# Kernel optimization log

Hardware: AMD Instinct MI355X
Metric: run time of the kernel (lower is better)

Reference implementation:

```python
import jax, jax.numpy as jnp
import numpy as np


def setup_inputs() -> dict:
    key = jax.random.key(0)
    ks = jax.random.split(key, 8)
    n_videos, emb_dim = 200000, 128
    n_nodes, k_neigh = 20000, 32
    sc = 1.0 / np.sqrt(emb_dim)
    return {
        "video_embeddings": jax.random.normal(ks[0], (n_videos, emb_dim), jnp.float32),
        "video_nodes": jax.random.randint(ks[1], (n_nodes,), 0, n_videos, jnp.int64 if jax.config.jax_enable_x64 else jnp.int32),
        "neigh_idx": jax.random.randint(ks[2], (n_nodes, k_neigh), 0, n_videos, jnp.int64 if jax.config.jax_enable_x64 else jnp.int32),
        "W1": jax.random.normal(ks[3], (2 * emb_dim, emb_dim), jnp.float32) * sc,
        "b1": jnp.zeros((emb_dim,), jnp.float32),
        "W2": jax.random.normal(ks[4], (emb_dim, emb_dim), jnp.float32) * sc,
        "b2": jnp.zeros((emb_dim,), jnp.float32),
        "W3": jax.random.normal(ks[5], (emb_dim, 1), jnp.float32) * sc,
        "b3": jnp.zeros((1,), jnp.float32),
    }


def reference(video_embeddings, video_nodes, neigh_idx, W1, b1, W2, b2, W3, b3):
    # Ragged per-node loop vectorized as a padded [N, K] neighbor gather.
    neigh_emb = video_embeddings[neigh_idx]          # [N, K, D]
    node_emb = video_embeddings[video_nodes]         # [N, D]
    n, k, d = neigh_emb.shape
    # Attention MLP: cat(neigh, node_repeated) -> relu -> relu -> scalar score
    x = jnp.concatenate([neigh_emb, jnp.broadcast_to(node_emb[:, None, :], (n, k, d))], axis=-1)  # [N, K, 2D]
    h = jax.nn.relu(jnp.einsum("nke,ed->nkd", x, W1) + b1)
    h = jax.nn.relu(jnp.einsum("nke,ed->nkd", h, W2) + b2)
    scores = (jnp.einsum("nkd,do->nko", h, W3) + b3)[..., 0]  # [N, K]
    att = jax.nn.softmax(scores, axis=-1)                      # softmax over neighbors
    # Weighted aggregation: embed_matrix[i] = neigh_emb[i].T @ att[i]
    return jnp.einsum("nkd,nk->nd", neigh_emb, att)
```

## Files before the change

### kernel.cpp

```cpp
#include <hip/hip_runtime.h>
#include <hip/hip_bf16.h>

#define D  128
#define KN 32
#define LST 136

typedef __attribute__((ext_vector_type(8))) short bf16x8;
typedef __attribute__((ext_vector_type(4))) float f32x4;

static __device__ __forceinline__ unsigned short f2bf(float f) {
    union { float f; unsigned int u; } v; v.f = f;
    unsigned int u = v.u;
    u += 0x7fff + ((u >> 16) & 1);
    return (unsigned short)(u >> 16);
}
static __device__ __forceinline__ float bf2f(unsigned short h) {
    union { float f; unsigned int u; } v; v.u = ((unsigned int)h) << 16;
    return v.f;
}
static __device__ __forceinline__ unsigned int pk2bf(float a, float b) {
    float2 t; t.x = a; t.y = b;
    __hip_bfloat162 h = __float22bfloat162_rn(t);
    union { __hip_bfloat162 h; unsigned int u; } v; v.h = h;
    return v.u;
}

__global__ __launch_bounds__(256) void wt_kernel(
    const float* __restrict__ W1, const float* __restrict__ W2,
    unsigned short* __restrict__ W1Tt, unsigned short* __restrict__ W1Tb,
    unsigned short* __restrict__ W2T)
{
    int idx = blockIdx.x * 256 + threadIdx.x;
    if (idx < D * D) {
        int col = idx >> 7, e = idx & 127;
        W1Tt[col * D + e] = f2bf(W1[e * D + col]);
        W1Tb[col * D + e] = f2bf(W1[(D + e) * D + col]);
        W2T [col * D + e] = f2bf(W2[e * D + col]);
    }
}

__global__ __launch_bounds__(256) void q_kernel(
    const float* __restrict__ emb, const int* __restrict__ vnodes, int NN,
    const unsigned short* __restrict__ W1Tb, const float* __restrict__ b1,
    float* __restrict__ Qf)
{
    __shared__ unsigned short sA[128][LST];

    const int tid  = threadIdx.x;
    const int lane = tid & 63;
    const int w    = tid >> 6;
    const int m    = lane & 15, q = lane >> 4;
    const int r0   = blockIdx.x * 128;

#pragma unroll
    for (int i = 0; i < 16; ++i) {
        int e = tid + 256 * i;
        int row = e >> 5, c4 = (e & 31) << 2;
        int r = r0 + row; if (r > NN - 1) r = NN - 1;
        int vr = vnodes[r];
        const float4 f = *(const float4*)(emb + (long)vr * D + c4);
        ushort4 h;
        h.x = f2bf(f.x); h.y = f2bf(f.y); h.z = f2bf(f.z); h.w = f2bf(f.w);
        *(ushort4*)(&sA[row][c4]) = h;
    }
    __syncthreads();

    bf16x8 Bf[2][4];
#pragma unroll
    for (int nt = 0; nt < 2; ++nt)
#pragma unroll
        for (int kk = 0; kk < 4; ++kk)
            Bf[nt][kk] = *(const bf16x8*)(W1Tb + (32 * w + 16 * nt + m) * D + kk * 32 + q * 8);
    float bv[2];
#pragma unroll
    for (int nt = 0; nt < 2; ++nt) bv[nt] = b1[32 * w + 16 * nt + m];

    f32x4 acc[8][2];
#pragma unroll
    for (int mt = 0; mt < 8; ++mt)
#pragma unroll
        for (int nt = 0; nt < 2; ++nt) acc[mt][nt] = (f32x4){0.f, 0.f, 0.f, 0.f};

#pragma unroll
    for (int kk = 0; kk < 4; ++kk)
#pragma unroll
        for (int mt = 0; mt < 8; ++mt) {
            bf16x8 a = *(const bf16x8*)(&sA[16 * mt + m][kk * 32 + q * 8]);
            acc[mt][0] = __builtin_amdgcn_mfma_f32_16x16x32_bf16(a, Bf[0][kk], acc[mt][0], 0, 0, 0);
            acc[mt][1] = __builtin_amdgcn_mfma_f32_16x16x32_bf16(a, Bf[1][kk], acc[mt][1], 0, 0, 0);
        }

#pragma unroll
    for (int mt = 0; mt < 8; ++mt)
#pragma unroll
        for (int nt = 0; nt < 2; ++nt) {
            int col = 32 * w + 16 * nt + m;
#pragma unroll
            for (int r = 0; r < 4; ++r) {
                int row = r0 + 16 * mt + 4 * q + r;
                if (row < NN) Qf[(long)row * D + col] = acc[mt][nt][r] + bv[nt];
            }
        }
}

__global__ __launch_bounds__(256, 3) void agg_kernel(
    const float* __restrict__ emb, const int* __restrict__ nidx,
    const unsigned short* __restrict__ W1Tt, const unsigned short* __restrict__ W2T,
    const float* __restrict__ b2, const float* __restrict__ W3,
    const float* __restrict__ b3, const float* __restrict__ Qf,
    float* __restrict__ out, int NN)
{
    __shared__ unsigned short sU[128][LST];
    __shared__ float sQf[4][D];
    __shared__ float sSp[4][128];
    __shared__ float sAtt[128];

    const int tid  = threadIdx.x;
    const int lane = tid & 63;
    const int w    = tid >> 6;
    const int m    = lane & 15, q = lane >> 4;

    bf16x8 Af[2][4], Bf[2][4];
#pragma unroll
    for (int t = 0; t < 2; ++t)
#pragma unroll
        for (int kk = 0; kk < 4; ++kk) {
            Af[t][kk] = *(const bf16x8*)(W1Tt + (32 * w + 16 * t + m) * D + kk * 32 + q * 8);
            Bf[t][kk] = *(const bf16x8*)(W2T  + (32 * w + 16 * t + m) * D + kk * 32 + q * 8);
        }
    float b2v[2], w3v[2];
#pragma unroll
    for (int nt = 0; nt < 2; ++nt) {
        int col = 32 * w + 16 * nt + m;
        b2v[nt] = b2[col];
        w3v[nt] = W3[col];
    }
    const float b3s = b3[0];

    const int groups = (NN + 3) >> 2;
    for (int g = blockIdx.x; g < groups; g += gridDim.x) {
        const int node0 = g * 4;

        {
            int i2 = tid * 2, nd = i2 >> 7, c = i2 & 127;
            int ndg = node0 + nd; if (ndg > NN - 1) ndg = NN - 1;
            *(float2*)(&sQf[nd][c]) = *(const float2*)(Qf + (long)ndg * D + c);
        }
        {
            int row = tid >> 1, half = tid & 1;
            int ndg = node0 + (row >> 5); if (ndg > NN - 1) ndg = NN - 1;
            int ni = nidx[ndg * KN + (row & 31)];
            const float* src = emb + (long)ni * D + half * 64;
#pragma unroll
            for (int j = 0; j < 8; ++j) {
                float4 f0 = *(const float4*)(src + j * 8);
                float4 f1 = *(const float4*)(src + j * 8 + 4);
                uint4 pk;
                pk.x = pk2bf(f0.x, f0.y); pk.y = pk2bf(f0.z, f0.w);
                pk.z = pk2bf(f1.x, f1.y); pk.w = pk2bf(f1.z, f1.w);
                *(uint4*)(&sU[row][half * 64 + j * 8]) = pk;
            }
        }
        __syncthreads();

        bf16x8 gv[8];
#pragma unroll
        for (int j = 0; j < 8; ++j)
            gv[j] = *(const bf16x8*)(&sU[w * KN + (lane >> 4) + 4 * j][(lane & 15) * 8]);

        f32x4 acc1[4][2][2];
#pragma unroll
        for (int nd = 0; nd < 4; ++nd)
#pragma unroll
            for (int t = 0; t < 2; ++t)
#pragma unroll
                for (int nt = 0; nt < 2; ++nt) acc1[nd][t][nt] = (f32x4){0.f, 0.f, 0.f, 0.f};

#pragma unroll
        for (int nd = 0; nd < 4; ++nd)
#pragma unroll
            for (int kk = 0; kk < 4; ++kk) {
                bf16x8 e0 = *(const bf16x8*)(&sU[nd * 32 + m][kk * 32 + q * 8]);
                bf16x8 e1 = *(const bf16x8*)(&sU[nd * 32 + 16 + m][kk * 32 + q * 8]);
                acc1[nd][0][0] = __builtin_amdgcn_mfma_f32_16x16x32_bf16(Af[0][kk], e0, acc1[nd][0][0], 0, 0, 0);
                acc1[nd][1][0] = __builtin_amdgcn_mfma_f32_16x16x32_bf16(Af[1][kk], e0, acc1[nd][1][0], 0, 0, 0);
                acc1[nd][0][1] = __builtin_amdgcn_mfma_f32_16x16x32_bf16(Af[0][kk], e1, acc1[nd][0][1], 0, 0, 0);
                acc1[nd][1][1] = __builtin_amdgcn_mfma_f32_16x16x32_bf16(Af[1][kk], e1, acc1[nd][1][1], 0, 0, 0);
            }
        __syncthreads();

#pragma unroll
        for (int nd = 0; nd < 4; ++nd)
#pragma unroll
            for (int t = 0; t < 2; ++t) {
                int xc = 32 * w + 16 * t + 4 * q;
                float q0 = sQf[nd][xc], q1 = sQf[nd][xc + 1];
                float q2 = sQf[nd][xc + 2], q3 = sQf[nd][xc + 3];
#pragma unroll
                for (int nt = 0; nt < 2; ++nt) {
                    float v0 = fmaxf(acc1[nd][t][nt][0] + q0, 0.f);
                    float v1 = fmaxf(acc1[nd][t][nt][1] + q1, 0.f);
                    float v2 = fmaxf(acc1[nd][t][nt][2] + q2, 0.f);
                    float v3 = fmaxf(acc1[nd][t][nt][3] + q3, 0.f);
                    uint2 pk; pk.x = pk2bf(v0, v1); pk.y = pk2bf(v2, v3);
                    *(uint2*)(&sU[nd * 32 + 16 * nt + m][xc]) = pk;
                }
            }
        __syncthreads();

        f32x4 acc[8][2];
#pragma unroll
        for (int mt = 0; mt < 8; ++mt)
#pragma unroll
            for (int nt = 0; nt < 2; ++nt) acc[mt][nt] = (f32x4){0.f, 0.f, 0.f, 0.f};

#pragma unroll
        for (int kk = 0; kk < 4; ++kk)
#pragma unroll
            for (int mt = 0; mt < 8; ++mt) {
                bf16x8 a = *(const bf16x8*)(&sU[16 * mt + m][kk * 32 + q * 8]);
                acc[mt][0] = __builtin_amdgcn_mfma_f32_16x16x32_bf16(a, Bf[0][kk], acc[mt][0], 0, 0, 0);
                acc[mt][1] = __builtin_amdgcn_mfma_f32_16x16x32_bf16(a, Bf[1][kk], acc[mt][1], 0, 0, 0);
            }

#pragma unroll
        for (int mt = 0; mt < 8; ++mt) {
            float p[4];
#pragma unroll
            for (int r = 0; r < 4; ++r) {
                float h0 = acc[mt][0][r] + b2v[0]; h0 = h0 > 0.f ? h0 : 0.f;
                float h1 = acc[mt][1][r] + b2v[1]; h1 = h1 > 0.f ? h1 : 0.f;
                p[r] = h0 * w3v[0] + h1 * w3v[1];
            }
#pragma unroll
            for (int off = 8; off >= 1; off >>= 1)
#pragma unroll
                for (int r = 0; r < 4; ++r) p[r] += __shfl_xor(p[r], off, 16);
            if (m == 0) {
#pragma unroll
                for (int r = 0; r < 4; ++r) sSp[w][16 * mt + 4 * q + r] = p[r];
            }
        }
        __syncthreads();

        if (tid < 128) {
            float s = sSp[0][tid] + sSp[1][tid] + sSp[2][tid] + sSp[3][tid] + b3s;
            float mx = s;
#pragma unroll
            for (int off = 16; off >= 1; off >>= 1) mx = fmaxf(mx, __shfl_xor(mx, off, 32));
            float e = __expf(s - mx);
            float sum = e;
#pragma unroll
            for (int off = 16; off >= 1; off >>= 1) sum += __shfl_xor(sum, off, 32);
            sAtt[tid] = e / sum;
        }
        __syncthreads();

        {
            float r[8] = {0.f, 0.f, 0.f, 0.f, 0.f, 0.f, 0.f, 0.f};
#pragma unroll
            for (int j = 0; j < 8; ++j) {
                float a = sAtt[w * KN + (lane >> 4) + 4 * j];
#pragma unroll
                for (int h = 0; h < 8; ++h)
                    r[h] += a * bf2f((unsigned short)gv[j][h]);
            }
#pragma unroll
            for (int h = 0; h < 8; ++h) {
                r[h] += __shfl_xor(r[h], 16);
                r[h] += __shfl_xor(r[h], 32);
            }
            int ndw = node0 + w;
            if (lane < 16 && ndw < NN) {
                float4 o0 = {r[0], r[1], r[2], r[3]};
                float4 o1 = {r[4], r[5], r[6], r[7]};
                *(float4*)(out + (long)ndw * D + lane * 8)     = o0;
                *(float4*)(out + (long)ndw * D + lane * 8 + 4) = o1;
            }
        }
    }
}

__global__ __launch_bounds__(128) void naive_kernel(
    const float* __restrict__ emb, const int* __restrict__ vnodes,
    const int* __restrict__ nidx,
    const float* __restrict__ W1, const float* __restrict__ b1,
    const float* __restrict__ W2, const float* __restrict__ b2,
    const float* __restrict__ W3, const float* __restrict__ b3,
    float* __restrict__ out)
{
    __shared__ float sE[KN + 1][D];
    __shared__ float sH[KN][D];
    __shared__ float sH2[KN][D];
    __shared__ float sS[KN];
    __shared__ float sA2[KN];
    const int node = blockIdx.x, tid = threadIdx.x;

    for (int r = 0; r < KN + 1; ++r) {
        int vr = (r < KN) ? nidx[node * KN + r] : vnodes[node];
        sE[r][tid] = emb[(long)vr * D + tid];
    }
    __syncthreads();
    for (int k = 0; k < KN; ++k) {
        float s = b1[tid];
        for (int e = 0; e < D; ++e) s += sE[k][e]  * W1[e * D + tid];
        for (int e = 0; e < D; ++e) s += sE[KN][e] * W1[(D + e) * D + tid];
        sH[k][tid] = s > 0.f ? s : 0.f;
    }
    __syncthreads();
    for (int k = 0; k < KN; ++k) {
        float s = b2[tid];
        for (int e = 0; e < D; ++e) s += sH[k][e] * W2[e * D + tid];
        sH2[k][tid] = s > 0.f ? s : 0.f;
    }
    __syncthreads();
    if (tid < KN) {
        float s = b3[0];
        for (int e = 0; e < D; ++e) s += sH2[tid][e] * W3[e];
        sS[tid] = s;
    }
    __syncthreads();
    if (tid == 0) {
        float mx = sS[0];
        for (int k = 1; k < KN; ++k) mx = fmaxf(mx, sS[k]);
        float sum = 0.f;
        for (int k = 0; k < KN; ++k) { sA2[k] = __expf(sS[k] - mx); sum += sA2[k]; }
        for (int k = 0; k < KN; ++k) sA2[k] /= sum;
    }
    __syncthreads();
    float a = 0.f;
    for (int k = 0; k < KN; ++k) a += sA2[k] * sE[k][tid];
    out[(long)node * D + tid] = a;
}

extern "C" void kernel_launch(void* const* d_in, const int* in_sizes, int n_in,
                              void* d_out, int out_size, void* d_ws, size_t ws_size,
                              hipStream_t stream) {
    const float* emb    = (const float*)d_in[0];
    const int*   vnodes = (const int*)d_in[1];
    const int*   nidx   = (const int*)d_in[2];
    const float* W1     = (const float*)d_in[3];
    const float* b1     = (const float*)d_in[4];
    const float* W2     = (const float*)d_in[5];
    const float* b2     = (const float*)d_in[6];
    const float* W3     = (const float*)d_in[7];
    const float* b3     = (const float*)d_in[8];
    float* out = (float*)d_out;

    const int NN = in_sizes[1];

    const size_t q_bytes  = (size_t)NN * D * sizeof(float);
    const size_t wt_elems = (size_t)D * D;
    const size_t need = q_bytes + 3 * wt_elems * sizeof(unsigned short);

    if (ws_size >= need) {
        float* Qf            = (float*)d_ws;
        unsigned short* W1Tt = (unsigned short*)((char*)d_ws + q_bytes);
        unsigned short* W1Tb = W1Tt + wt_elems;
        unsigned short* W2T  = W1Tb + wt_elems;

        wt_kernel<<<(D * D + 255) / 256, 256, 0, stream>>>(W1, W2, W1Tt, W1Tb, W2T);
        q_kernel<<<(NN + 127) / 128, 256, 0, stream>>>(emb, vnodes, NN, W1Tb, b1, Qf);
        agg_kernel<<<2048, 256, 0, stream>>>(
            emb, nidx, W1Tt, W2T, b2, W3, b3, Qf, out, NN);
    } else {
        naive_kernel<<<NN, D, 0, stream>>>(emb, vnodes, nidx, W1, b1, W2, b2, W3, b3, out);
    }
}
```

Baseline: 336.0 us.

## Process two nodes per block iteration with separate gather and hidden LDS buffers

The aggregation kernel now handles 2 nodes (64 neighbour rows) per loop iteration instead of 4. It keeps the gathered embeddings in their own LDS buffer and writes the layer-1 output to a second buffer, which removes one barrier and the register copy of the gathered rows. The final weighted sum is done by 128 threads reading straight from LDS, and the grid is doubled. The b3 bias is dropped because softmax does not change when a constant is added. Smaller LDS and register use should allow more resident blocks, at the cost of more loop iterations and an extra barrier at the end of each one.

```diff
diff --git a/kernel.cpp b/kernel.cpp
--- a/kernel.cpp
+++ b/kernel.cpp
@@ -14,9 +14,11 @@
     u += 0x7fff + ((u >> 16) & 1);
     return (unsigned short)(u >> 16);
 }
-static __device__ __forceinline__ float bf2f(unsigned short h) {
-    union { float f; unsigned int u; } v; v.u = ((unsigned int)h) << 16;
-    return v.f;
+static __device__ __forceinline__ float bflo(unsigned int u) {
+    union { float f; unsigned int u; } v; v.u = u << 16; return v.f;
+}
+static __device__ __forceinline__ float bfhi(unsigned int u) {
+    union { float f; unsigned int u; } v; v.u = u & 0xffff0000u; return v.f;
 }
 static __device__ __forceinline__ unsigned int pk2bf(float a, float b) {
     float2 t; t.x = a; t.y = b;
@@ -107,13 +109,14 @@
     const float* __restrict__ emb, const int* __restrict__ nidx,
     const unsigned short* __restrict__ W1Tt, const unsigned short* __restrict__ W2T,
     const float* __restrict__ b2, const float* __restrict__ W3,
-    const float* __restrict__ b3, const float* __restrict__ Qf,
+    const float* __restrict__ Qf,
     float* __restrict__ out, int NN)
 {
-    __shared__ unsigned short sU[128][LST];
-    __shared__ float sQf[4][D];
-    __shared__ float sSp[4][128];
-    __shared__ float sAtt[128];
+    __shared__ unsigned short sEg[64][LST];
+    __shared__ unsigned short sX[64][LST];
+    __shared__ float sQf[2][D];
+    __shared__ float sSp[4][64];
+    __shared__ float sAtt[64];
 
     const int tid  = threadIdx.x;
     const int lane = tid & 63;
@@ -135,116 +138,121 @@
         b2v[nt] = b2[col];
         w3v[nt] = W3[col];
     }
-    const float b3s = b3[0];
-
-    const int groups = (NN + 3) >> 2;
+
+    const int groups = (NN + 1) >> 1;
     for (int g = blockIdx.x; g < groups; g += gridDim.x) {
-        const int node0 = g * 4;
+        const int node0 = g * 2;
 
         {
-            int i2 = tid * 2, nd = i2 >> 7, c = i2 & 127;
+            int nd = tid >> 7, c = tid & 127;
             int ndg = node0 + nd; if (ndg > NN - 1) ndg = NN - 1;
-            *(float2*)(&sQf[nd][c]) = *(const float2*)(Qf + (long)ndg * D + c);
+            sQf[nd][c] = Qf[(long)ndg * D + c];
         }
         {
-            int row = tid >> 1, half = tid & 1;
+            int row = tid >> 2, qt = tid & 3;
             int ndg = node0 + (row >> 5); if (ndg > NN - 1) ndg = NN - 1;
             int ni = nidx[ndg * KN + (row & 31)];
-            const float* src = emb + (long)ni * D + half * 64;
-#pragma unroll
-            for (int j = 0; j < 8; ++j) {
-                float4 f0 = *(const float4*)(src + j * 8);
-                float4 f1 = *(const float4*)(src + j * 8 + 4);
-                uint4 pk;
-                pk.x = pk2bf(f0.x, f0.y); pk.y = pk2bf(f0.z, f0.w);
-                pk.z = pk2bf(f1.x, f1.y); pk.w = pk2bf(f1.z, f1.w);
-                *(uint4*)(&sU[row][half * 64 + j * 8]) = pk;
-            }
-        }
-        __syncthreads();
-
-        bf16x8 gv[8];
-#pragma unroll
-        for (int j = 0; j < 8; ++j)
-            gv[j] = *(const bf16x8*)(&sU[w * KN + (lane >> 4) + 4 * j][(lane & 15) * 8]);
-
-        f32x4 acc1[4][2][2];
-#pragma unroll
-        for (int nd = 0; nd < 4; ++nd)
+            const float* src = emb + (long)ni * D + qt * 32;
+            float4 f0 = *(const float4*)(src);
+            float4 f1 = *(const float4*)(src + 4);
+            float4 f2 = *(const float4*)(src + 8);
+            float4 f3 = *(const float4*)(src + 12);
+            float4 f4 = *(const float4*)(src + 16);
+            float4 f5 = *(const float4*)(src + 20);
+            float4 f6 = *(const float4*)(src + 24);
+            float4 f7 = *(const float4*)(src + 28);
+            uint4 p0, p1;
+            p0.x = pk2bf(f0.x, f0.y); p0.y = pk2bf(f0.z, f0.w);
+            p0.z = pk2bf(f1.x, f1.y); p0.w = pk2bf(f1.z, f1.w);
+            p1.x = pk2bf(f2.x, f2.y); p1.y = pk2bf(f2.z, f2.w);
+            p1.z = pk2bf(f3.x, f3.y); p1.w = pk2bf(f3.z, f3.w);
+            *(uint4*)(&sEg[row][qt * 32])     = p0;
+            *(uint4*)(&sEg[row][qt * 32 + 8]) = p1;
+            uint4 p2, p3;
+            p2.x = pk2bf(f4.x, f4.y); p2.y = pk2bf(f4.z, f4.w);
+            p2.z = pk2bf(f5.x, f5.y); p2.w = pk2bf(f5.z, f5.w);
+            p3.x = pk2bf(f6.x, f6.y); p3.y = pk2bf(f6.z, f6.w);
+            p3.z = pk2bf(f7.x, f7.y); p3.w = pk2bf(f7.z, f7.w);
+            *(uint4*)(&sEg[row][qt * 32 + 16]) = p2;
+            *(uint4*)(&sEg[row][qt * 32 + 24]) = p3;
+        }
+        __syncthreads();
+
+        {
+            f32x4 acc1[2][4];
 #pragma unroll
             for (int t = 0; t < 2; ++t)
 #pragma unroll
-                for (int nt = 0; nt < 2; ++nt) acc1[nd][t][nt] = (f32x4){0.f, 0.f, 0.f, 0.f};
-
-#pragma unroll
-        for (int nd = 0; nd < 4; ++nd)
-#pragma unroll
-            for (int kk = 0; kk < 4; ++kk) {
-                bf16x8 e0 = *(const bf16x8*)(&sU[nd * 32 + m][kk * 32 + q * 8]);
-                bf16x8 e1 = *(const bf16x8*)(&sU[nd * 32 + 16 + m][kk * 32 + q * 8]);
-                acc1[nd][0][0] = __builtin_amdgcn_mfma_f32_16x16x32_bf16(Af[0][kk], e0, acc1[nd][0][0], 0, 0, 0);
-                acc1[nd][1][0] = __builtin_amdgcn_mfma_f32_16x16x32_bf16(Af[1][kk], e0, acc1[nd][1][0], 0, 0, 0);
-                acc1[nd][0][1] = __builtin_amdgcn_mfma_f32_16x16x32_bf16(Af[0][kk], e1, acc1[nd][0][1], 0, 0, 0);
-                acc1[nd][1][1] = __builtin_amdgcn_mfma_f32_16x16x32_bf16(Af[1][kk], e1, acc1[nd][1][1], 0, 0, 0);
-            }
-        __syncthreads();
-
-#pragma unroll
-        for (int nd = 0; nd < 4; ++nd)
+                for (int nt = 0; nt < 4; ++nt) acc1[t][nt] = (f32x4){0.f, 0.f, 0.f, 0.f};
+
+#pragma unroll
+            for (int kk = 0; kk < 4; ++kk)
+#pragma unroll
+                for (int nt = 0; nt < 4; ++nt) {
+                    bf16x8 e = *(const bf16x8*)(&sEg[16 * nt + m][kk * 32 + q * 8]);
+                    acc1[0][nt] = __builtin_amdgcn_mfma_f32_16x16x32_bf16(Af[0][kk], e, acc1[0][nt], 0, 0, 0);
+                    acc1[1][nt] = __builtin_amdgcn_mfma_f32_16x16x32_bf16(Af[1][kk], e, acc1[1][nt], 0, 0, 0);
+                }
+
 #pragma unroll
             for (int t = 0; t < 2; ++t) {
                 int xc = 32 * w + 16 * t + 4 * q;
-                float q0 = sQf[nd][xc], q1 = sQf[nd][xc + 1];
-                float q2 = sQf[nd][xc + 2], q3 = sQf[nd][xc + 3];
-#pragma unroll
-                for (int nt = 0; nt < 2; ++nt) {
-                    float v0 = fmaxf(acc1[nd][t][nt][0] + q0, 0.f);
-                    float v1 = fmaxf(acc1[nd][t][nt][1] + q1, 0.f);
-                    float v2 = fmaxf(acc1[nd][t][nt][2] + q2, 0.f);
-                    float v3 = fmaxf(acc1[nd][t][nt][3] + q3, 0.f);
+                float q0[4];
+#pragma unroll
+                for (int nt = 0; nt < 4; ++nt) {
+                    int n = 16 * nt + m;
+                    int nd = n >> 5;
+                    float v0 = fmaxf(acc1[t][nt][0] + sQf[nd][xc],     0.f);
+                    float v1 = fmaxf(acc1[t][nt][1] + sQf[nd][xc + 1], 0.f);
+                    float v2 = fmaxf(acc1[t][nt][2] + sQf[nd][xc + 2], 0.f);
+                    float v3 = fmaxf(acc1[t][nt][3] + sQf[nd][xc + 3], 0.f);
                     uint2 pk; pk.x = pk2bf(v0, v1); pk.y = pk2bf(v2, v3);
-                    *(uint2*)(&sU[nd * 32 + 16 * nt + m][xc]) = pk;
-                }
-            }
-        __syncthreads();
-
-        f32x4 acc[8][2];
-#pragma unroll
-        for (int mt = 0; mt < 8; ++mt)
-#pragma unroll
-            for (int nt = 0; nt < 2; ++nt) acc[mt][nt] = (f32x4){0.f, 0.f, 0.f, 0.f};
-
-#pragma unroll
-        for (int kk = 0; kk < 4; ++kk)
-#pragma unroll
-            for (int mt = 0; mt < 8; ++mt) {
-                bf16x8 a = *(const bf16x8*)(&sU[16 * mt + m][kk * 32 + q * 8]);
-                acc[mt][0] = __builtin_amdgcn_mfma_f32_16x16x32_bf16(a, Bf[0][kk], acc[mt][0], 0, 0, 0);
-                acc[mt][1] = __builtin_amdgcn_mfma_f32_16x16x32_bf16(a, Bf[1][kk], acc[mt][1], 0, 0, 0);
-            }
-
-#pragma unroll
-        for (int mt = 0; mt < 8; ++mt) {
-            float p[4];
-#pragma unroll
-            for (int r = 0; r < 4; ++r) {
-                float h0 = acc[mt][0][r] + b2v[0]; h0 = h0 > 0.f ? h0 : 0.f;
-                float h1 = acc[mt][1][r] + b2v[1]; h1 = h1 > 0.f ? h1 : 0.f;
-                p[r] = h0 * w3v[0] + h1 * w3v[1];
-            }
-#pragma unroll
-            for (int off = 8; off >= 1; off >>= 1)
-#pragma unroll
-                for (int r = 0; r < 4; ++r) p[r] += __shfl_xor(p[r], off, 16);
-            if (m == 0) {
-#pragma unroll
-                for (int r = 0; r < 4; ++r) sSp[w][16 * mt + 4 * q + r] = p[r];
-            }
-        }
-        __syncthreads();
-
-        if (tid < 128) {
-            float s = sSp[0][tid] + sSp[1][tid] + sSp[2][tid] + sSp[3][tid] + b3s;
+                    *(uint2*)(&sX[n][xc]) = pk;
+                }
+                (void)q0;
+            }
+        }
+        __syncthreads();
+
+        {
+            f32x4 acc[4][2];
+#pragma unroll
+            for (int mt = 0; mt < 4; ++mt)
+#pragma unroll
+                for (int nt = 0; nt < 2; ++nt) acc[mt][nt] = (f32x4){0.f, 0.f, 0.f, 0.f};
+
+#pragma unroll
+            for (int kk = 0; kk < 4; ++kk)
+#pragma unroll
+                for (int mt = 0; mt < 4; ++mt) {
+                    bf16x8 a = *(const bf16x8*)(&sX[16 * mt + m][kk * 32 + q * 8]);
+                    acc[mt][0] = __builtin_amdgcn_mfma_f32_16x16x32_bf16(a, Bf[0][kk], acc[mt][0], 0, 0, 0);
+                    acc[mt][1] = __builtin_amdgcn_mfma_f32_16x16x32_bf16(a, Bf[1][kk], acc[mt][1], 0, 0, 0);
+                }
+
+#pragma unroll
+            for (int mt = 0; mt < 4; ++mt) {
+                float p[4];
+#pragma unroll
+                for (int r = 0; r < 4; ++r) {
+                    float h0 = acc[mt][0][r] + b2v[0]; h0 = h0 > 0.f ? h0 : 0.f;
+                    float h1 = acc[mt][1][r] + b2v[1]; h1 = h1 > 0.f ? h1 : 0.f;
+                    p[r] = h0 * w3v[0] + h1 * w3v[1];
+                }
+#pragma unroll
+                for (int off = 8; off >= 1; off >>= 1)
+#pragma unroll
+                    for (int r = 0; r < 4; ++r) p[r] += __shfl_xor(p[r], off, 16);
+                if (m == 0) {
+#pragma unroll
+                    for (int r = 0; r < 4; ++r) sSp[w][16 * mt + 4 * q + r] = p[r];
+                }
+            }
+        }
+        __syncthreads();
+
+        if (tid < 64) {
+            float s = sSp[0][tid] + sSp[1][tid] + sSp[2][tid] + sSp[3][tid];
             float mx = s;
 #pragma unroll
             for (int off = 16; off >= 1; off >>= 1) mx = fmaxf(mx, __shfl_xor(mx, off, 32));
@@ -256,28 +264,23 @@
         }
         __syncthreads();
 
-        {
-            float r[8] = {0.f, 0.f, 0.f, 0.f, 0.f, 0.f, 0.f, 0.f};
-#pragma unroll
-            for (int j = 0; j < 8; ++j) {
-                float a = sAtt[w * KN + (lane >> 4) + 4 * j];
-#pragma unroll
-                for (int h = 0; h < 8; ++h)
-                    r[h] += a * bf2f((unsigned short)gv[j][h]);
-            }
-#pragma unroll
-            for (int h = 0; h < 8; ++h) {
-                r[h] += __shfl_xor(r[h], 16);
-                r[h] += __shfl_xor(r[h], 32);
-            }
-            int ndw = node0 + w;
-            if (lane < 16 && ndw < NN) {
-                float4 o0 = {r[0], r[1], r[2], r[3]};
-                float4 o1 = {r[4], r[5], r[6], r[7]};
-                *(float4*)(out + (long)ndw * D + lane * 8)     = o0;
-                *(float4*)(out + (long)ndw * D + lane * 8 + 4) = o1;
-            }
-        }
+        if (tid < 128) {
+            int nd = tid >> 6, c2 = tid & 63;
+            float ox = 0.f, oy = 0.f;
+#pragma unroll
+            for (int k = 0; k < KN; ++k) {
+                float a = sAtt[nd * KN + k];
+                unsigned int v = *(const unsigned int*)(&sEg[nd * KN + k][c2 * 2]);
+                ox += a * bflo(v);
+                oy += a * bfhi(v);
+            }
+            int ndg = node0 + nd;
+            if (ndg < NN) {
+                float2 o = {ox, oy};
+                *(float2*)(out + (long)ndg * D + c2 * 2) = o;
+            }
+        }
+        __syncthreads();
     }
 }
 
@@ -361,8 +364,8 @@
 
         wt_kernel<<<(D * D + 255) / 256, 256, 0, stream>>>(W1, W2, W1Tt, W1Tb, W2T);
         q_kernel<<<(NN + 127) / 128, 256, 0, stream>>>(emb, vnodes, NN, W1Tb, b1, Qf);
-        agg_kernel<<<2048, 256, 0, stream>>>(
-            emb, nidx, W1Tt, W2T, b2, W3, b3, Qf, out, NN);
+        agg_kernel<<<4096, 256, 0, stream>>>(
+            emb, nidx, W1Tt, W2T, b2, W3, Qf, out, NN);
     } else {
         naive_kernel<<<NN, D, 0, stream>>>(emb, vnodes, nidx, W1, b1, W2, b2, W3, b3, out);
     }
```

After: 373.4 us. 11.1% more time.
